# Optimization experiments

Measured on AMD Instinct MI355X. Metric: run time of the kernel, lower is better.

The kernel has to match this reference:

```python
import jax, jax.numpy as jnp
import numpy as np

N_NODES = 50000
N_EDGES = 1600000
F_IN = 256
HID = 256
HEADS = 8
HD = HID // HEADS  # 32
SLOPE = 0.2
EPS = 1e-5


def setup_inputs() -> dict:
    key = jax.random.key(0)
    ks = jax.random.split(key, 10)
    node_features = jax.random.normal(ks[0], (N_NODES, F_IN), jnp.float32)
    edge_index = jax.random.randint(ks[1], (2, N_EDGES), 0, N_NODES, jnp.int32)
    s = 1.0 / np.sqrt(F_IN)
    W = jax.random.uniform(ks[2], (HEADS, F_IN, HD), jnp.float32, -s, s)
    bw = jax.random.uniform(ks[3], (HEADS, HD), jnp.float32, -s, s)
    sa = 1.0 / np.sqrt(2 * HD)
    A = jax.random.uniform(ks[4], (HEADS, 2 * HD), jnp.float32, -sa, sa)
    ba = jax.random.uniform(ks[5], (HEADS,), jnp.float32, -sa, sa)
    gamma = jnp.ones((HEADS, HD), jnp.float32)
    beta = jnp.zeros((HEADS, HD), jnp.float32)
    so = 1.0 / np.sqrt(HD)
    Wout = jax.random.uniform(ks[6], (HD, HID), jnp.float32, -so, so)
    bout = jax.random.uniform(ks[7], (HID,), jnp.float32, -so, so)
    return dict(node_features=node_features, edge_index=edge_index, W=W, bw=bw,
                A=A, ba=ba, gamma=gamma, beta=beta, Wout=Wout, bout=bout)


def _head(x, W, bw, a, ba, gamma, beta, tgt, src):
    h = x @ W + bw                         # [N, d]
    # attn(concat(h_i, h_j)) = h_i @ a1 + h_j @ a2 + ba  (linear over concat)
    si = h @ a[:HD]                        # [N]
    sj = h @ a[HD:]                        # [N]
    e = si[tgt] + sj[src] + ba             # [E]
    e = jnp.where(e >= 0, e, SLOPE * e)    # leaky_relu
    # scatter_softmax over edges grouped by target node (stable)
    m = jax.ops.segment_max(e, tgt, num_segments=N_NODES)
    ex = jnp.exp(e - m[tgt])
    den = jax.ops.segment_sum(ex, tgt, num_segments=N_NODES)
    alpha = ex / den[tgt]                  # [E]  (dropout in eval mode = identity)
    msg = alpha[:, None] * h[src]          # [E, d]
    agg = jax.ops.segment_sum(msg, tgt, num_segments=N_NODES)  # [N, d]
    out = agg + h                          # skip connection
    out = jnp.where(out > 0, out, jnp.expm1(out))  # ELU
    mu = out.mean(axis=-1, keepdims=True)
    var = out.var(axis=-1, keepdims=True)
    return (out - mu) * jax.lax.rsqrt(var + EPS) * gamma + beta


def reference(node_features, edge_index, W, bw, A, ba, gamma, beta, Wout, bout):
    tgt = edge_index[0]
    src = edge_index[1]
    heads = jax.vmap(_head, in_axes=(None, 0, 0, 0, 0, 0, 0, None, None))(
        node_features, W, bw, A, ba, gamma, beta, tgt, src)   # [H, N, d]
    mean = heads.mean(axis=0)                                  # [N, d]
    y = mean @ Wout + bout                                     # [N, HID]
    return jnp.where(y > 0, y, jnp.expm1(y))                   # ELU
```

## Files before the change

### kernel.cpp

```cpp
#include <hip/hip_runtime.h>
#include <hip/hip_bf16.h>
#include <hip/hip_fp16.h>

#define N_NODES 50000
#define N_EDGES 1600000
#define HEADS 8
#define HD 32
#define FIN 256
#define HID 256

typedef unsigned short u16;
typedef unsigned int u32;

typedef short s8v __attribute__((ext_vector_type(8)));
typedef float f4v __attribute__((ext_vector_type(4)));
typedef float fx4 __attribute__((ext_vector_type(4)));

__device__ __forceinline__ u32 pk2(float lo, float hi) {
  __hip_bfloat162 b = __float22bfloat162_rn(make_float2(lo, hi));
  union { __hip_bfloat162 b2; u32 u; } c;
  c.b2 = b;
  return c.u;
}

__global__ __launch_bounds__(256) void k_prepw(const float* __restrict__ W,
                                               u16* __restrict__ Wp) {
  int id = blockIdx.x * 256 + threadIdx.x;
  int col = id >> 8;
  int k = id & 255;
  int h = col >> 5, d = col & 31;
  Wp[col * 256 + k] = (u16)(pk2(W[h * 8192 + k * 32 + d], 0.f) & 0xFFFFu);
}

__global__ __launch_bounds__(512) void k_gemm(
    const float* __restrict__ X, const u16* __restrict__ Wp,
    const float* __restrict__ bw, const float* __restrict__ A,
    __half* __restrict__ Hb, float* __restrict__ si, float* __restrict__ sj) {
  __shared__ __align__(16) u16 Xs[128 * 40];
  __shared__ __align__(16) u16 Wt[256 * 40];

  const int t = threadIdx.x;
  const int m0 = blockIdx.x * 128;
  const int w = t >> 6;
  const int lane = t & 63;
  const int l15 = lane & 15;
  const int quad = lane >> 4;
  const int wm = (w >> 2) * 64;
  const int wn = (w & 3) * 64;

  f4v acc[4][4];
#pragma unroll
  for (int i = 0; i < 4; i++)
#pragma unroll
    for (int j = 0; j < 4; j++) acc[i][j] = (f4v){0.f, 0.f, 0.f, 0.f};

  const int wcol = t >> 2;
  const int wpart = t & 3;

  for (int k0 = 0; k0 < FIN; k0 += 32) {
#pragma unroll
    for (int p = 0; p < 2; p++) {
      int row = p * 64 + (t >> 3);
      int f4 = t & 7;
      int node = m0 + row;
      fx4 xv = (fx4){0.f, 0.f, 0.f, 0.f};
      if (node < N_NODES)
        xv = __builtin_nontemporal_load((const fx4*)&X[node * FIN + k0 + f4 * 4]);
      u32* dst = (u32*)&Xs[row * 40 + f4 * 4];
      dst[0] = pk2(xv[0], xv[1]);
      dst[1] = pk2(xv[2], xv[3]);
    }
#pragma unroll
    for (int c2 = 0; c2 < 2; c2++) {
      int cc = wcol + c2 * 128;
      *(fx4*)&Wt[cc * 40 + wpart * 8] =
          *(const fx4*)&Wp[cc * 256 + k0 + wpart * 8];
    }
    __syncthreads();
    s8v af[4], bf[4];
#pragma unroll
    for (int mi = 0; mi < 4; mi++)
      af[mi] = *(const s8v*)&Xs[(wm + mi * 16 + l15) * 40 + quad * 8];
#pragma unroll
    for (int ni = 0; ni < 4; ni++)
      bf[ni] = *(const s8v*)&Wt[(wn + ni * 16 + l15) * 40 + quad * 8];
#pragma unroll
    for (int mi = 0; mi < 4; mi++)
#pragma unroll
      for (int ni = 0; ni < 4; ni++)
        acc[mi][ni] = __builtin_amdgcn_mfma_f32_16x16x32_bf16(af[mi], bf[ni], acc[mi][ni], 0, 0, 0);
    __syncthreads();
  }

  const int head0 = wn >> 5;
  const int head1 = head0 + 1;
  float c1a0 = A[head0 * 64 + l15],      c1a1 = A[head0 * 64 + 16 + l15];
  float c2a0 = A[head0 * 64 + 32 + l15], c2a1 = A[head0 * 64 + 48 + l15];
  float c1b0 = A[head1 * 64 + l15],      c1b1 = A[head1 * 64 + 16 + l15];
  float c2b0 = A[head1 * 64 + 32 + l15], c2b1 = A[head1 * 64 + 48 + l15];

#pragma unroll
  for (int mi = 0; mi < 4; mi++) {
#pragma unroll
    for (int ni = 0; ni < 4; ni++) {
      float b = bw[wn + ni * 16 + l15];
#pragma unroll
      for (int r = 0; r < 4; r++) acc[mi][ni][r] += b;
    }
    const int rbase = m0 + wm + mi * 16 + quad * 4;
#pragma unroll
    for (int r = 0; r < 4; r++) {
      int node = rbase + r;
      if (node < N_NODES) {
#pragma unroll
        for (int ni = 0; ni < 4; ni++) {
          int col = wn + ni * 16 + l15;
          Hb[node * HID + col] = __float2half_rn(acc[mi][ni][r]);
        }
      }
    }
    float s1a[4], s2a[4], s1b[4], s2b[4];
#pragma unroll
    for (int r = 0; r < 4; r++) {
      s1a[r] = acc[mi][0][r] * c1a0 + acc[mi][1][r] * c1a1;
      s2a[r] = acc[mi][0][r] * c2a0 + acc[mi][1][r] * c2a1;
      s1b[r] = acc[mi][2][r] * c1b0 + acc[mi][3][r] * c1b1;
      s2b[r] = acc[mi][2][r] * c2b0 + acc[mi][3][r] * c2b1;
    }
#pragma unroll
    for (int off = 1; off <= 8; off <<= 1) {
#pragma unroll
      for (int r = 0; r < 4; r++) {
        s1a[r] += __shfl_xor(s1a[r], off);
        s2a[r] += __shfl_xor(s2a[r], off);
        s1b[r] += __shfl_xor(s1b[r], off);
        s2b[r] += __shfl_xor(s2b[r], off);
      }
    }
    if (l15 == 0) {
#pragma unroll
      for (int r = 0; r < 4; r++) {
        int node = rbase + r;
        if (node < N_NODES) {
          si[node * HEADS + head0] = s1a[r];
          sj[node * HEADS + head0] = s2a[r];
          si[node * HEADS + head1] = s1b[r];
          sj[node * HEADS + head1] = s2b[r];
        }
      }
    }
  }
}

__global__ void k_hist(const int* __restrict__ tgt, int* __restrict__ cnt,
                       int* __restrict__ rank) {
  int e = blockIdx.x * 256 + threadIdx.x;
  if (e < N_EDGES) rank[e] = atomicAdd(&cnt[tgt[e]], 1);
}

__global__ __launch_bounds__(256) void k_scan1(const int* __restrict__ cnt,
    int* __restrict__ excl, int* __restrict__ bsum) {
  __shared__ int s[256];
  const int t = threadIdx.x;
  const int i = blockIdx.x * 256 + t;
  int v = (i < N_NODES) ? cnt[i] : 0;
  s[t] = v;
  __syncthreads();
  int x = v;
  for (int off = 1; off < 256; off <<= 1) {
    int y = (t >= off) ? s[t - off] : 0;
    __syncthreads();
    x += y;
    s[t] = x;
    __syncthreads();
  }
  if (i < N_NODES) excl[i] = x - v;
  if (t == 255) bsum[blockIdx.x] = x;
}

__global__ __launch_bounds__(256) void k_scan2(const int* __restrict__ bsum,
                                               int* __restrict__ boff) {
  __shared__ int s[256];
  const int t = threadIdx.x;
  int v = (t < 196) ? bsum[t] : 0;
  s[t] = v;
  __syncthreads();
  int x = v;
  for (int off = 1; off < 256; off <<= 1) {
    int y = (t >= off) ? s[t - off] : 0;
    __syncthreads();
    x += y;
    s[t] = x;
    __syncthreads();
  }
  if (t < 196) boff[t] = x - v;
}

__global__ void k_scan3(const int* __restrict__ excl, const int* __restrict__ boff,
                        int* __restrict__ rowptr) {
  int i = blockIdx.x * 256 + threadIdx.x;
  if (i < N_NODES) rowptr[i] = excl[i] + boff[blockIdx.x];
}

__global__ void k_scatter(const int* __restrict__ tgt, const int* __restrict__ src,
                          const int* __restrict__ rowptr, const int* __restrict__ rank,
                          int* __restrict__ sortedSrc) {
  int e = blockIdx.x * 256 + threadIdx.x;
  if (e < N_EDGES) sortedSrc[rowptr[tgt[e]] + rank[e]] = src[e];
}

__global__ void k_dhist(const int* __restrict__ cnt, int* __restrict__ dcnt) {
  int n = blockIdx.x * 256 + threadIdx.x;
  if (n < N_NODES) atomicAdd(&dcnt[255 - min(cnt[n], 255)], 1);
}

__global__ __launch_bounds__(256) void k_dscan(const int* __restrict__ dcnt,
                                               int* __restrict__ dcur) {
  __shared__ int s[256];
  const int t = threadIdx.x;
  int v = dcnt[t];
  s[t] = v;
  __syncthreads();
  int x = v;
  for (int off = 1; off < 256; off <<= 1) {
    int y = (t >= off) ? s[t - off] : 0;
    __syncthreads();
    x += y;
    s[t] = x;
    __syncthreads();
  }
  dcur[t] = x - v;
}

__global__ void k_dscatter(const int* __restrict__ cnt, int* __restrict__ dcur,
                           int* __restrict__ perm) {
  int n = blockIdx.x * 256 + threadIdx.x;
  if (n < N_NODES) {
    int pos = atomicAdd(&dcur[255 - min(cnt[n], 255)], 1);
    perm[pos] = n;
  }
}

__global__ __launch_bounds__(256) void k_fused(
    const __half* __restrict__ Hb, const float* __restrict__ si,
    const float* __restrict__ sj, const float* __restrict__ ba,
    const float* __restrict__ gamma, const float* __restrict__ beta,
    const float* __restrict__ Wout, const float* __restrict__ bout,
    const int* __restrict__ rowptr, const int* __restrict__ cnt,
    const int* __restrict__ sortedSrc, const int* __restrict__ perm,
    float* __restrict__ out) {
  const int t = threadIdx.x;
  const int lane = t & 63;
  const int n = perm[blockIdx.x * 4 + (t >> 6)];
  const int cg = lane & 31;
  const int es = lane >> 5;
  const int hh = cg >> 2;
  const int start = rowptr[n];
  const int deg = cnt[n];

  const float sb = si[n * HEADS + hh] + ba[hh];
  const char* hbBase = (const char*)Hb + 16 * cg;
  const int* ss = sortedSrc + start;

  float acc[8] = {0.f, 0.f, 0.f, 0.f, 0.f, 0.f, 0.f, 0.f};
  float den = 0.f;
#pragma unroll 4
  for (int slot = es; slot < deg; slot += 2) {
    int s = __builtin_nontemporal_load(ss + slot);
    float e = sb + sj[s * HEADS + hh];
    e = (e >= 0.f) ? e : 0.2f * e;
    float exv = __expf(e);
    float4 hb4 = *(const float4*)(hbBase + (size_t)s * (HID * 2));
    const __half2* hp = (const __half2*)&hb4;
#pragma unroll
    for (int d = 0; d < 4; d++) {
      acc[2 * d]     += exv * __low2float(hp[d]);
      acc[2 * d + 1] += exv * __high2float(hp[d]);
    }
    den += exv;
  }
#pragma unroll
  for (int j = 0; j < 8; j++) acc[j] += __shfl_xor(acc[j], 32);
  den += __shfl_xor(den, 32);

  float4 h4 = *(const float4*)((const char*)Hb + (size_t)n * (HID * 2) + 16 * cg);
  const __half2* hq = (const __half2*)&h4;
  float inv = (deg > 0) ? __fdividef(1.f, den) : 0.f;
  float v[8], sum = 0.f, sq = 0.f;
#pragma unroll
  for (int j = 0; j < 8; j++) {
    float hv = (j & 1) ? __high2float(hq[j >> 1]) : __low2float(hq[j >> 1]);
    float x = acc[j] * inv + hv;
    x = (x > 0.f) ? x : (__expf(x) - 1.f);
    v[j] = x;
    sum += x;
    sq += x * x;
  }
  sum += __shfl_xor(sum, 1); sq += __shfl_xor(sq, 1);
  sum += __shfl_xor(sum, 2); sq += __shfl_xor(sq, 2);
  float mu = sum * (1.f / 32.f);
  float var = sq * (1.f / 32.f) - mu * mu;
  float rstd = rsqrtf(var + 1e-5f);
  fx4 g0 = *(const fx4*)&gamma[cg * 8];
  fx4 g1 = *(const fx4*)&gamma[cg * 8 + 4];
  fx4 b0 = *(const fx4*)&beta[cg * 8];
  fx4 b1 = *(const fx4*)&beta[cg * 8 + 4];
  float m2[8];
#pragma unroll
  for (int j = 0; j < 8; j++) {
    float g = (j < 4) ? g0[j] : g1[j - 4];
    float bb = (j < 4) ? b0[j] : b1[j - 4];
    m2[j] = (v[j] - mu) * rstd * g + bb;
  }
#pragma unroll
  for (int j = 0; j < 8; j++) {
    m2[j] += __shfl_xor(m2[j], 4);
    m2[j] += __shfl_xor(m2[j], 8);
    m2[j] += __shfl_xor(m2[j], 16);
  }
  fx4 y = *(const fx4*)&bout[4 * lane];
#pragma unroll
  for (int q = 0; q < 4; q++) {
    float mv[8];
#pragma unroll
    for (int j = 0; j < 8; j++) mv[j] = __shfl(m2[j], q) * 0.125f;
#pragma unroll
    for (int j = 0; j < 8; j++) {
      fx4 w4 = *(const fx4*)&Wout[(q * 8 + j) * HID + 4 * lane];
      y += mv[j] * w4;
    }
  }
#pragma unroll
  for (int c = 0; c < 4; c++) y[c] = (y[c] > 0.f) ? y[c] : (__expf(y[c]) - 1.f);
  __builtin_nontemporal_store(y, (fx4*)&out[(size_t)n * HID + 4 * lane]);
}

extern "C" void kernel_launch(void* const* d_in, const int* in_sizes, int n_in,
                              void* d_out, int out_size, void* d_ws, size_t ws_size,
                              hipStream_t stream) {
  const float* X     = (const float*)d_in[0];
  const int*   EI    = (const int*)d_in[1];
  const float* W     = (const float*)d_in[2];
  const float* bw    = (const float*)d_in[3];
  const float* A     = (const float*)d_in[4];
  const float* ba    = (const float*)d_in[5];
  const float* gamma = (const float*)d_in[6];
  const float* beta  = (const float*)d_in[7];
  const float* Wout  = (const float*)d_in[8];
  const float* bout  = (const float*)d_in[9];
  float* out = (float*)d_out;
  const int* tgt = EI;
  const int* src = EI + N_EDGES;

  char* ws = (char*)d_ws;
  size_t off = 0;
  auto alloc = [&](size_t bytes) -> void* {
    void* p = ws + off;
    off += bytes;
    off = (off + 255) & ~(size_t)255;
    return p;
  };
  __half* Hb       = (__half*)alloc((size_t)N_NODES * HID * 2);
  float* si        = (float*)alloc((size_t)N_NODES * HEADS * 4);
  float* sj        = (float*)alloc((size_t)N_NODES * HEADS * 4);
  int*   cnt       = (int*)  alloc((size_t)N_NODES * 4);
  int*   excl      = (int*)  alloc((size_t)N_NODES * 4);
  int*   bsum      = (int*)  alloc(256 * 4);
  int*   boff      = (int*)  alloc(256 * 4);
  int*   rowptr    = (int*)  alloc((size_t)N_NODES * 4);
  int*   rank      = (int*)  alloc((size_t)N_EDGES * 4);
  int*   sortedSrc = (int*)  alloc((size_t)N_EDGES * 4);
  int*   dcnt      = (int*)  alloc(256 * 4);
  int*   dcur      = (int*)  alloc(256 * 4);
  int*   perm      = (int*)  alloc((size_t)N_NODES * 4);
  u16*   Wp        = (u16*)  alloc((size_t)HID * FIN * 2);

  hipMemsetAsync(cnt, 0, (size_t)N_NODES * 4, stream);
  hipMemsetAsync(dcnt, 0, 256 * 4, stream);
  k_prepw<<<256, 256, 0, stream>>>(W, Wp);
  k_hist<<<(N_EDGES + 255) / 256, 256, 0, stream>>>(tgt, cnt, rank);
  k_scan1<<<196, 256, 0, stream>>>(cnt, excl, bsum);
  k_scan2<<<1, 256, 0, stream>>>(bsum, boff);
  k_scan3<<<196, 256, 0, stream>>>(excl, boff, rowptr);
  k_scatter<<<(N_EDGES + 255) / 256, 256, 0, stream>>>(tgt, src, rowptr, rank, sortedSrc);
  k_dhist<<<196, 256, 0, stream>>>(cnt, dcnt);
  k_dscan<<<1, 256, 0, stream>>>(dcnt, dcur);
  k_dscatter<<<196, 256, 0, stream>>>(cnt, dcur, perm);
  k_gemm<<<(N_NODES + 127) / 128, 512, 0, stream>>>(X, Wp, bw, A, Hb, si, sj);
  k_fused<<<(N_NODES + 3) / 4, 256, 0, stream>>>(Hb, si, sj, ba, gamma, beta,
                                                 Wout, bout, rowptr, cnt,
                                                 sortedSrc, perm, out);
}
```

Measured before the change: 588.6 us.

## Collapse CSR scan into one single-block kernel and drop degree-sorted node permutation

Replaces the three-kernel prefix scan with one 1024-thread block that scans chunks of 49 counts serially and writes rowptr directly. Removes the degree-histogram, scan and scatter kernels that built a degree-descending node permutation, so the fused kernel now walks nodes in natural order. Adds nontemporal loads for the edge index streams. This cuts kernel launches and intermediate buffers, but gives up degree-sorted load balancing and runs the scan on a single workgroup with strided per-thread reads.

```diff
diff --git a/kernel.cpp b/kernel.cpp
--- a/kernel.cpp
+++ b/kernel.cpp
@@ -155,89 +155,54 @@
 __global__ void k_hist(const int* __restrict__ tgt, int* __restrict__ cnt,
                        int* __restrict__ rank) {
   int e = blockIdx.x * 256 + threadIdx.x;
-  if (e < N_EDGES) rank[e] = atomicAdd(&cnt[tgt[e]], 1);
-}
-
-__global__ __launch_bounds__(256) void k_scan1(const int* __restrict__ cnt,
-    int* __restrict__ excl, int* __restrict__ bsum) {
-  __shared__ int s[256];
+  if (e < N_EDGES) {
+    int tg = __builtin_nontemporal_load(tgt + e);
+    rank[e] = atomicAdd(&cnt[tg], 1);
+  }
+}
+
+#define SCHUNK 49
+__global__ __launch_bounds__(1024) void k_scan(const int* __restrict__ cnt,
+                                               int* __restrict__ rowptr) {
+  __shared__ int s[1024];
   const int t = threadIdx.x;
-  const int i = blockIdx.x * 256 + t;
-  int v = (i < N_NODES) ? cnt[i] : 0;
-  s[t] = v;
+  const int base = t * SCHUNK;
+  int sum = 0;
+#pragma unroll 7
+  for (int j = 0; j < SCHUNK; j++) {
+    int i = base + j;
+    sum += (i < N_NODES) ? cnt[i] : 0;
+  }
+  s[t] = sum;
   __syncthreads();
-  int x = v;
-  for (int off = 1; off < 256; off <<= 1) {
+  int x = sum;
+  for (int off = 1; off < 1024; off <<= 1) {
     int y = (t >= off) ? s[t - off] : 0;
     __syncthreads();
     x += y;
     s[t] = x;
     __syncthreads();
   }
-  if (i < N_NODES) excl[i] = x - v;
-  if (t == 255) bsum[blockIdx.x] = x;
-}
-
-__global__ __launch_bounds__(256) void k_scan2(const int* __restrict__ bsum,
-                                               int* __restrict__ boff) {
-  __shared__ int s[256];
-  const int t = threadIdx.x;
-  int v = (t < 196) ? bsum[t] : 0;
-  s[t] = v;
-  __syncthreads();
-  int x = v;
-  for (int off = 1; off < 256; off <<= 1) {
-    int y = (t >= off) ? s[t - off] : 0;
-    __syncthreads();
-    x += y;
-    s[t] = x;
-    __syncthreads();
-  }
-  if (t < 196) boff[t] = x - v;
-}
-
-__global__ void k_scan3(const int* __restrict__ excl, const int* __restrict__ boff,
-                        int* __restrict__ rowptr) {
-  int i = blockIdx.x * 256 + threadIdx.x;
-  if (i < N_NODES) rowptr[i] = excl[i] + boff[blockIdx.x];
+  int run = x - sum;
+#pragma unroll 7
+  for (int j = 0; j < SCHUNK; j++) {
+    int i = base + j;
+    if (i < N_NODES) {
+      rowptr[i] = run;
+      run += cnt[i];
+    }
+  }
 }
 
 __global__ void k_scatter(const int* __restrict__ tgt, const int* __restrict__ src,
                           const int* __restrict__ rowptr, const int* __restrict__ rank,
                           int* __restrict__ sortedSrc) {
   int e = blockIdx.x * 256 + threadIdx.x;
-  if (e < N_EDGES) sortedSrc[rowptr[tgt[e]] + rank[e]] = src[e];
-}
-
-__global__ void k_dhist(const int* __restrict__ cnt, int* __restrict__ dcnt) {
-  int n = blockIdx.x * 256 + threadIdx.x;
-  if (n < N_NODES) atomicAdd(&dcnt[255 - min(cnt[n], 255)], 1);
-}
-
-__global__ __launch_bounds__(256) void k_dscan(const int* __restrict__ dcnt,
-                                               int* __restrict__ dcur) {
-  __shared__ int s[256];
-  const int t = threadIdx.x;
-  int v = dcnt[t];
-  s[t] = v;
-  __syncthreads();
-  int x = v;
-  for (int off = 1; off < 256; off <<= 1) {
-    int y = (t >= off) ? s[t - off] : 0;
-    __syncthreads();
-    x += y;
-    s[t] = x;
-    __syncthreads();
-  }
-  dcur[t] = x - v;
-}
-
-__global__ void k_dscatter(const int* __restrict__ cnt, int* __restrict__ dcur,
-                           int* __restrict__ perm) {
-  int n = blockIdx.x * 256 + threadIdx.x;
-  if (n < N_NODES) {
-    int pos = atomicAdd(&dcur[255 - min(cnt[n], 255)], 1);
-    perm[pos] = n;
+  if (e < N_EDGES) {
+    int tg = __builtin_nontemporal_load(tgt + e);
+    int sc = __builtin_nontemporal_load(src + e);
+    int rk = __builtin_nontemporal_load(rank + e);
+    sortedSrc[rowptr[tg] + rk] = sc;
   }
 }
 
@@ -247,11 +212,10 @@
     const float* __restrict__ gamma, const float* __restrict__ beta,
     const float* __restrict__ Wout, const float* __restrict__ bout,
     const int* __restrict__ rowptr, const int* __restrict__ cnt,
-    const int* __restrict__ sortedSrc, const int* __restrict__ perm,
-    float* __restrict__ out) {
+    const int* __restrict__ sortedSrc, float* __restrict__ out) {
   const int t = threadIdx.x;
   const int lane = t & 63;
-  const int n = perm[blockIdx.x * 4 + (t >> 6)];
+  const int n = blockIdx.x * 4 + (t >> 6);
   const int cg = lane & 31;
   const int es = lane >> 5;
   const int hh = cg >> 2;
@@ -364,30 +328,18 @@
   float* si        = (float*)alloc((size_t)N_NODES * HEADS * 4);
   float* sj        = (float*)alloc((size_t)N_NODES * HEADS * 4);
   int*   cnt       = (int*)  alloc((size_t)N_NODES * 4);
-  int*   excl      = (int*)  alloc((size_t)N_NODES * 4);
-  int*   bsum      = (int*)  alloc(256 * 4);
-  int*   boff      = (int*)  alloc(256 * 4);
   int*   rowptr    = (int*)  alloc((size_t)N_NODES * 4);
   int*   rank      = (int*)  alloc((size_t)N_EDGES * 4);
   int*   sortedSrc = (int*)  alloc((size_t)N_EDGES * 4);
-  int*   dcnt      = (int*)  alloc(256 * 4);
-  int*   dcur      = (int*)  alloc(256 * 4);
-  int*   perm      = (int*)  alloc((size_t)N_NODES * 4);
   u16*   Wp        = (u16*)  alloc((size_t)HID * FIN * 2);
 
   hipMemsetAsync(cnt, 0, (size_t)N_NODES * 4, stream);
-  hipMemsetAsync(dcnt, 0, 256 * 4, stream);
   k_prepw<<<256, 256, 0, stream>>>(W, Wp);
   k_hist<<<(N_EDGES + 255) / 256, 256, 0, stream>>>(tgt, cnt, rank);
-  k_scan1<<<196, 256, 0, stream>>>(cnt, excl, bsum);
-  k_scan2<<<1, 256, 0, stream>>>(bsum, boff);
-  k_scan3<<<196, 256, 0, stream>>>(excl, boff, rowptr);
+  k_scan<<<1, 1024, 0, stream>>>(cnt, rowptr);
   k_scatter<<<(N_EDGES + 255) / 256, 256, 0, stream>>>(tgt, src, rowptr, rank, sortedSrc);
-  k_dhist<<<196, 256, 0, stream>>>(cnt, dcnt);
-  k_dscan<<<1, 256, 0, stream>>>(dcnt, dcur);
-  k_dscatter<<<196, 256, 0, stream>>>(cnt, dcur, perm);
   k_gemm<<<(N_NODES + 127) / 128, 512, 0, stream>>>(X, Wp, bw, A, Hb, si, sj);
   k_fused<<<(N_NODES + 3) / 4, 256, 0, stream>>>(Hb, si, sj, ba, gamma, beta,
                                                  Wout, bout, rowptr, cnt,
-                                                 sortedSrc, perm, out);
-}
+                                                 sortedSrc, out);
+}
```

New measurement: 494.2 us. -16.0%, faster.
